# Kernel tuning notes

Measured on AMD Instinct MI355X. Metric: run time of the kernel, lower is better.

Reference implementation:

```python
import jax, jax.numpy as jnp
import numpy as np

B, H, D, E, K = 4096, 1024, 4096, 8, 2


def setup_inputs() -> dict:
    key = jax.random.key(0)
    ks = jax.random.split(key, 7)
    s = 0.02
    return {
        "x": jax.random.normal(ks[0], (B, H), dtype=jnp.float32),
        "gate_w": jax.random.normal(ks[1], (H, E), dtype=jnp.float32) * s,
        "gate_b": jnp.zeros((E,), dtype=jnp.float32),
        "w1": jax.random.normal(ks[2], (E, H, D), dtype=jnp.float32) * s,
        "b1": jnp.zeros((E, D), dtype=jnp.float32),
        "w2": jax.random.normal(ks[3], (E, D, H), dtype=jnp.float32) * s,
        "b2": jnp.zeros((E, H), dtype=jnp.float32),
    }


def reference(x, gate_w, gate_b, w1, b1, w2, b2):
    # Gating: softmax over experts, top-k routing (Switch-style, k=2 here).
    logits = x @ gate_w + gate_b                      # [B, E]
    probs = jax.nn.softmax(logits, axis=-1)           # [B, E]
    topk_vals, topk_idx = jax.lax.top_k(probs, K)     # [B, K]

    # Routing mask: token b routed to expert e iff e in its top-k.
    onehot = jax.nn.one_hot(topk_idx, E, dtype=probs.dtype)  # [B, K, E]
    routed = onehot.max(axis=1)                        # [B, E] in {0,1}

    # Dense per-expert MLPs (grouped GEMM form), then masked scaled combine.
    # h: [E, B, D]; out: [E, B, H]
    h = jax.nn.relu(jnp.einsum('bh,ehd->ebd', x, w1) + b1[:, None, :])
    out = jnp.einsum('ebd,edh->ebh', h, w2) + b2[:, None, :]
    scale = (probs * routed / K).T                     # [E, B]
    y = jnp.einsum('ebh,eb->bh', out, scale)           # [B, H]

    # Switch-style load-balancing aux loss.
    prob_per_expert = probs.mean(axis=0)               # [E]
    tokens_per_expert = routed.mean(axis=0)            # [E]
    aux_loss = (prob_per_expert * tokens_per_expert).sum() * E
    return (y, aux_loss)
```

## Files before the change

### kernel.cpp

```cpp
#include <hip/hip_runtime.h>
#include <stdint.h>
#include <math.h>

typedef unsigned short u16;
typedef __attribute__((ext_vector_type(4))) unsigned short u16x4;
typedef __attribute__((ext_vector_type(8))) short short8;
typedef __attribute__((ext_vector_type(4))) float floatx4;

#define B_TOK 4096
#define H_DIM 1024
#define D_DIM 4096
#define E_NUM 8
#define PAIR_CAP 9216
#define GATE_BLOCKS 256


__device__ __forceinline__ u16 f2bf(float f) {
  union { float f; uint32_t u; } v; v.f = f;
  uint32_t r = (v.u + 0x7fffu + ((v.u >> 16) & 1u)) >> 16;
  return (u16)r;
}

__device__ __forceinline__ void gload_lds16(const u16* g, u16* l) {
  __builtin_amdgcn_global_load_lds((const __attribute__((address_space(1))) void*)g,
                                   (__attribute__((address_space(3))) void*)l, 16, 0, 0);
}


__global__ __launch_bounds__(256) void gate_kernel(
    const float* __restrict__ x, const float* __restrict__ gw, const float* __restrict__ gb,
    int* __restrict__ pcnt, float* __restrict__ psum,
    int* __restrict__ tidx, float* __restrict__ tscale) {
  int wave = threadIdx.x >> 6, lane = threadIdx.x & 63;
  __shared__ int scnt[4][8];
  __shared__ float ssum[4][8];
  int lcnt[8] = {0,0,0,0,0,0,0,0};
  float lsum[8] = {0.f,0.f,0.f,0.f,0.f,0.f,0.f,0.f};

  for (int it = 0; it < 4; it++) {
    int b = blockIdx.x * 16 + it * 4 + wave;
    const float* xr = x + (size_t)b * H_DIM;
    float acc[8] = {0.f,0.f,0.f,0.f,0.f,0.f,0.f,0.f};
    for (int i = 0; i < 16; i++) {
      int h = lane + i * 64;
      float xv = xr[h];
      const float* g = gw + h * 8;
      #pragma unroll
      for (int e = 0; e < 8; e++) acc[e] += xv * g[e];
    }
    #pragma unroll
    for (int e = 0; e < 8; e++) {
      #pragma unroll
      for (int off = 32; off > 0; off >>= 1) acc[e] += __shfl_down(acc[e], off);
    }
    if (lane == 0) {
      float p[8], m = -1e30f, s = 0.f;
      #pragma unroll
      for (int e = 0; e < 8; e++) { p[e] = acc[e] + gb[e]; m = fmaxf(m, p[e]); }
      #pragma unroll
      for (int e = 0; e < 8; e++) { p[e] = expf(p[e] - m); s += p[e]; }
      float inv = 1.f / s;
      #pragma unroll
      for (int e = 0; e < 8; e++) { p[e] *= inv; lsum[e] += p[e]; }
      int i1 = 0;
      #pragma unroll
      for (int e = 1; e < 8; e++) if (p[e] > p[i1]) i1 = e;
      int i2 = (i1 == 0) ? 1 : 0;
      #pragma unroll
      for (int e = 0; e < 8; e++) if (e != i1 && p[e] > p[i2]) i2 = e;
      tidx[2*b]     = i1; tscale[2*b]     = p[i1] * 0.5f;
      tidx[2*b + 1] = i2; tscale[2*b + 1] = p[i2] * 0.5f;
      lcnt[i1]++; lcnt[i2]++;
    }
  }
  if (lane == 0) {
    #pragma unroll
    for (int e = 0; e < 8; e++) { scnt[wave][e] = lcnt[e]; ssum[wave][e] = lsum[e]; }
  }
  __syncthreads();
  if (threadIdx.x < 8) {
    int e = threadIdx.x;
    int c = scnt[0][e] + scnt[1][e] + scnt[2][e] + scnt[3][e];
    float s = ssum[0][e] + ssum[1][e] + ssum[2][e] + ssum[3][e];
    pcnt[blockIdx.x * 8 + e] = c;
    psum[blockIdx.x * 8 + e] = s;
  }
}


__global__ __launch_bounds__(256) void offsets_kernel(
    const int* __restrict__ pcnt, const float* __restrict__ psum,
    int* __restrict__ offs, int* __restrict__ ptok,
    float* __restrict__ pscale, float* __restrict__ aux_out) {
  __shared__ int cnt[8];
  __shared__ float ps[8];
  if (threadIdx.x < 8) {
    int e = threadIdx.x;
    int c = 0; float s = 0.f;
    for (int i = 0; i < GATE_BLOCKS; i++) { c += pcnt[i * 8 + e]; s += psum[i * 8 + e]; }
    cnt[e] = c; ps[e] = s;
  }
  __syncthreads();
  if (threadIdx.x == 0) {
    int o = 0;
    float aux = 0.f;
    for (int e = 0; e < 8; e++) {
      offs[e] = o;
      o += ((cnt[e] + 127) >> 7) << 7;
      aux += (ps[e] * (1.f / 4096.f)) * ((float)cnt[e] * (1.f / 4096.f));
    }
    offs[8] = o;
    aux_out[0] = aux * 8.f;
  }
  for (int i = threadIdx.x; i < PAIR_CAP; i += 256) { ptok[i] = 0; pscale[i] = 0.f; }
}


__global__ __launch_bounds__(256) void scatter_kernel(
    const int* __restrict__ tidx, const float* __restrict__ tscale,
    const int* __restrict__ offs, int* __restrict__ fill,
    int* __restrict__ ptok, float* __restrict__ pscale) {
  __shared__ int lcnt[8];
  __shared__ int lbase[8];
  if (threadIdx.x < 8) lcnt[threadIdx.x] = 0;
  __syncthreads();
  int b = blockIdx.x * 256 + threadIdx.x;
  int e0 = tidx[2*b], e1 = tidx[2*b + 1];
  int p0 = atomicAdd(&lcnt[e0], 1);
  int p1 = atomicAdd(&lcnt[e1], 1);
  __syncthreads();
  if (threadIdx.x < 8) {
    int e = threadIdx.x;
    lbase[e] = offs[e] + atomicAdd(&fill[e], lcnt[e]);
  }
  __syncthreads();
  int pos0 = lbase[e0] + p0;
  int pos1 = lbase[e1] + p1;
  ptok[pos0] = b; pscale[pos0] = tscale[2*b];
  ptok[pos1] = b; pscale[pos1] = tscale[2*b + 1];
}


__global__ __launch_bounds__(256) void convert_x(const float* __restrict__ in, u16* __restrict__ out) {
  int i = blockIdx.x * 256 + threadIdx.x;
  float4 v = ((const float4*)in)[i];
  u16x4 o;
  o[0] = f2bf(v.x); o[1] = f2bf(v.y); o[2] = f2bf(v.z); o[3] = f2bf(v.w);
  ((u16x4*)out)[i] = o;
}


__global__ __launch_bounds__(256) void transpose_convert(
    const float* __restrict__ in, u16* __restrict__ out, int R, int C) {
  __shared__ u16 tile[64 * 65];
  size_t eoff = (size_t)blockIdx.z * R * C;
  const float* inp = in + eoff;
  u16* outp = out + eoff;
  int c0 = blockIdx.x * 64, r0 = blockIdx.y * 64;
  int t = threadIdx.x;
  int rr = t >> 4, cc = t & 15;
  #pragma unroll
  for (int p = 0; p < 4; p++) {
    int r = rr + p * 16;
    float4 v = *(const float4*)(inp + (size_t)(r0 + r) * C + c0 + cc * 4);
    int base = r * 65 + cc * 4;
    tile[base + 0] = f2bf(v.x); tile[base + 1] = f2bf(v.y);
    tile[base + 2] = f2bf(v.z); tile[base + 3] = f2bf(v.w);
  }
  __syncthreads();
  #pragma unroll
  for (int p = 0; p < 4; p++) {
    int c = rr + p * 16;
    u16x4 w;
    w[0] = tile[(cc*4 + 0) * 65 + c];
    w[1] = tile[(cc*4 + 1) * 65 + c];
    w[2] = tile[(cc*4 + 2) * 65 + c];
    w[3] = tile[(cc*4 + 3) * 65 + c];
    *(u16x4*)(outp + (size_t)(c0 + c) * R + r0 + cc * 4) = w;
  }
}


template <bool FIRST>
__global__ __launch_bounds__(256, 2) void moe_gemm(
    const u16* __restrict__ A, const u16* __restrict__ Bw, const float* __restrict__ bias,
    const int* __restrict__ ptok, const float* __restrict__ pscale,
    const int* __restrict__ offs, u16* __restrict__ Hout, float* __restrict__ Y) {
  constexpr int KD = FIRST ? H_DIM : D_DIM;
  constexpr int ND = FIRST ? D_DIM : H_DIM;
  constexpr int AS = FIRST ? H_DIM : D_DIM;

  const int row0 = blockIdx.y * 128;
  const int total = offs[8];
  if (row0 >= total) return;
  int e = 0;
  #pragma unroll
  for (int q = 0; q < 7; q++) if (row0 >= offs[q + 1]) e = q + 1;

  const int n0 = blockIdx.x * 128;
  const int t = threadIdx.x;

  __shared__ __align__(16) u16 lA[128 * 32];
  __shared__ __align__(16) u16 lB[128 * 32];

  const int rA0 = row0 + (t >> 2);
  const int rA1 = rA0 + 64;
  size_t aoff0, aoff1;
  if (FIRST) {
    aoff0 = (size_t)ptok[rA0] * AS;
    aoff1 = (size_t)ptok[rA1] * AS;
  } else {
    aoff0 = (size_t)rA0 * AS;
    aoff1 = (size_t)rA1 * AS;
  }
  const u16* gA0 = A + aoff0 + (t & 3) * 8;
  const u16* gA1 = A + aoff1 + (t & 3) * 8;
  const u16* Be = Bw + (size_t)e * (H_DIM * D_DIM);
  const u16* gB0 = Be + (size_t)(n0 + (t >> 2)) * KD + (t & 3) * 8;
  const u16* gB1 = gB0 + (size_t)64 * KD;
  u16* dA0 = &lA[t * 8];       u16* dA1 = &lA[(t + 256) * 8];
  u16* dB0 = &lB[t * 8];       u16* dB1 = &lB[(t + 256) * 8];

  const int wave = t >> 6, lane = t & 63;
  const int wr = (wave >> 1) * 64, wc = (wave & 1) * 64;
  const int fr = lane & 15, fg = lane >> 4;

  floatx4 acc[4][4];
  #pragma unroll
  for (int i = 0; i < 4; i++)
    #pragma unroll
    for (int j = 0; j < 4; j++) acc[i][j] = (floatx4){0.f, 0.f, 0.f, 0.f};

  for (int k0 = 0; k0 < KD; k0 += 32) {
    gload_lds16(gA0 + k0, dA0);
    gload_lds16(gA1 + k0, dA1);
    gload_lds16(gB0 + k0, dB0);
    gload_lds16(gB1 + k0, dB1);
    __syncthreads();
    short8 af[4], bf[4];
    #pragma unroll
    for (int i = 0; i < 4; i++) af[i] = *(const short8*)&lA[(wr + i * 16 + fr) * 32 + fg * 8];
    #pragma unroll
    for (int j = 0; j < 4; j++) bf[j] = *(const short8*)&lB[(wc + j * 16 + fr) * 32 + fg * 8];
    #pragma unroll
    for (int i = 0; i < 4; i++)
      #pragma unroll
      for (int j = 0; j < 4; j++)
        acc[i][j] = __builtin_amdgcn_mfma_f32_16x16x32_bf16(af[i], bf[j], acc[i][j], 0, 0, 0);
    __syncthreads();
  }

  if (FIRST) {
    const float* be = bias + (size_t)e * ND;
    #pragma unroll
    for (int i = 0; i < 4; i++) {
      #pragma unroll
      for (int r = 0; r < 4; r++) {
        int row = row0 + wr + i * 16 + fg * 4 + r;
        u16* hrow = Hout + (size_t)row * ND;
        #pragma unroll
        for (int j = 0; j < 4; j++) {
          int col = n0 + wc + j * 16 + fr;
          float v = acc[i][j][r] + be[col];
          hrow[col] = f2bf(fmaxf(v, 0.f));
        }
      }
    }
  } else {
    const float* be = bias + (size_t)e * ND;
    #pragma unroll
    for (int i = 0; i < 4; i++) {
      #pragma unroll
      for (int r = 0; r < 4; r++) {
        int row = row0 + wr + i * 16 + fg * 4 + r;
        float sc = pscale[row];
        if (sc != 0.f) {
          int tok = ptok[row];
          float* yrow = Y + (size_t)tok * ND;
          #pragma unroll
          for (int j = 0; j < 4; j++) {
            int col = n0 + wc + j * 16 + fr;
            atomicAdd(&yrow[col], (acc[i][j][r] + be[col]) * sc);
          }
        }
      }
    }
  }
}


extern "C" void kernel_launch(void* const* d_in, const int* in_sizes, int n_in,
                              void* d_out, int out_size, void* d_ws, size_t ws_size,
                              hipStream_t stream) {
  const float* x      = (const float*)d_in[0];
  const float* gate_w = (const float*)d_in[1];
  const float* gate_b = (const float*)d_in[2];
  const float* w1     = (const float*)d_in[3];
  const float* b1     = (const float*)d_in[4];
  const float* w2     = (const float*)d_in[5];
  const float* b2     = (const float*)d_in[6];
  float* out = (float*)d_out;

  char* ws = (char*)d_ws;
  u16*   x_bf   = (u16*)  (ws);
  u16*   w1t    = (u16*)  (ws + 8388608);
  u16*   w2t    = (u16*)  (ws + 75497472);
  u16*   h_bf   = (u16*)  (ws + 142606336);
  int*   ptok   = (int*)  (ws + 218103808);
  float* pscale = (float*)(ws + 218140672);
  int*   tidx   = (int*)  (ws + 218177536);
  float* tscale = (float*)(ws + 218210304);
  int*   ctr    = (int*)  (ws + 218243072);
  int*   fill     = ctr;
  int*   offs     = ctr + 8;
  int*   pcnt     = ctr + 32;
  float* psum     = (float*)(ctr + 32 + GATE_BLOCKS * 8);

  hipMemsetAsync(d_out, 0, (size_t)out_size * sizeof(float), stream);
  hipMemsetAsync(fill, 0, 8 * sizeof(int), stream);

  convert_x<<<(B_TOK * H_DIM) / 4 / 256, 256, 0, stream>>>(x, x_bf);
  transpose_convert<<<dim3(D_DIM / 64, H_DIM / 64, E_NUM), 256, 0, stream>>>(w1, w1t, H_DIM, D_DIM);
  transpose_convert<<<dim3(H_DIM / 64, D_DIM / 64, E_NUM), 256, 0, stream>>>(w2, w2t, D_DIM, H_DIM);
  gate_kernel<<<GATE_BLOCKS, 256, 0, stream>>>(x, gate_w, gate_b, pcnt, psum, tidx, tscale);
  offsets_kernel<<<1, 256, 0, stream>>>(pcnt, psum, offs, ptok, pscale, out + (size_t)B_TOK * H_DIM);
  scatter_kernel<<<B_TOK / 256, 256, 0, stream>>>(tidx, tscale, offs, fill, ptok, pscale);
  moe_gemm<true><<<dim3(D_DIM / 128, PAIR_CAP / 128), 256, 0, stream>>>(
      x_bf, w1t, b1, ptok, pscale, offs, h_bf, nullptr);
  moe_gemm<false><<<dim3(H_DIM / 128, PAIR_CAP / 128), 256, 0, stream>>>(
      h_bf, w2t, b2, ptok, pscale, offs, nullptr, out);
}
```

Baseline: 617.7 us.

## Split-K second GEMM into per-pair partials, add swizzled LDS, deterministic combine

The second expert GEMM now splits K into two halves across blockIdx.z and writes plain fp32 partial results per routed pair into a workspace buffer, rather than doing scaled atomicAdds into the output. A new combine kernel gathers each token's two pairs and both K-halves, adds the bias and applies the routing scales. This doubles the grid for the small-N second GEMM and removes the atomics and the output memset. An XOR swizzle on the LDS tile column is also added to cut bank conflicts in both GEMMs. The cost is extra partial-buffer traffic, about 75MB written and read back, which reuses the x_bf/w1t region of the workspace.

```diff
diff --git a/kernel.cpp b/kernel.cpp
--- a/kernel.cpp
+++ b/kernel.cpp
@@ -90,8 +90,7 @@
 
 __global__ __launch_bounds__(256) void offsets_kernel(
     const int* __restrict__ pcnt, const float* __restrict__ psum,
-    int* __restrict__ offs, int* __restrict__ ptok,
-    float* __restrict__ pscale, float* __restrict__ aux_out) {
+    int* __restrict__ offs, int* __restrict__ ptok, float* __restrict__ aux_out) {
   __shared__ int cnt[8];
   __shared__ float ps[8];
   if (threadIdx.x < 8) {
@@ -112,14 +111,15 @@
     offs[8] = o;
     aux_out[0] = aux * 8.f;
   }
-  for (int i = threadIdx.x; i < PAIR_CAP; i += 256) { ptok[i] = 0; pscale[i] = 0.f; }
+  for (int i = threadIdx.x; i < PAIR_CAP; i += 256) ptok[i] = 0;
 }
 
 
 __global__ __launch_bounds__(256) void scatter_kernel(
     const int* __restrict__ tidx, const float* __restrict__ tscale,
     const int* __restrict__ offs, int* __restrict__ fill,
-    int* __restrict__ ptok, float* __restrict__ pscale) {
+    int* __restrict__ ptok, float* __restrict__ pscale,
+    int* __restrict__ pexp, int* __restrict__ pairpos) {
   __shared__ int lcnt[8];
   __shared__ int lbase[8];
   if (threadIdx.x < 8) lcnt[threadIdx.x] = 0;
@@ -136,8 +136,8 @@
   __syncthreads();
   int pos0 = lbase[e0] + p0;
   int pos1 = lbase[e1] + p1;
-  ptok[pos0] = b; pscale[pos0] = tscale[2*b];
-  ptok[pos1] = b; pscale[pos1] = tscale[2*b + 1];
+  ptok[pos0] = b; pscale[pos0] = tscale[2*b];     pexp[pos0] = e0; pairpos[2*b]     = pos0;
+  ptok[pos1] = b; pscale[pos1] = tscale[2*b + 1]; pexp[pos1] = e1; pairpos[2*b + 1] = pos1;
 }
 
 
@@ -184,9 +184,10 @@
 template <bool FIRST>
 __global__ __launch_bounds__(256, 2) void moe_gemm(
     const u16* __restrict__ A, const u16* __restrict__ Bw, const float* __restrict__ bias,
-    const int* __restrict__ ptok, const float* __restrict__ pscale,
-    const int* __restrict__ offs, u16* __restrict__ Hout, float* __restrict__ Y) {
+    const int* __restrict__ ptok, const int* __restrict__ offs,
+    u16* __restrict__ Hout, float* __restrict__ Y) {
   constexpr int KD = FIRST ? H_DIM : D_DIM;
+  constexpr int KSPAN = FIRST ? KD : KD / 2;
   constexpr int ND = FIRST ? D_DIM : H_DIM;
   constexpr int AS = FIRST ? H_DIM : D_DIM;
 
@@ -199,6 +200,7 @@
 
   const int n0 = blockIdx.x * 128;
   const int t = threadIdx.x;
+  const int kbase = FIRST ? 0 : (int)blockIdx.z * KSPAN;
 
   __shared__ __align__(16) u16 lA[128 * 32];
   __shared__ __align__(16) u16 lB[128 * 32];
@@ -213,10 +215,11 @@
     aoff0 = (size_t)rA0 * AS;
     aoff1 = (size_t)rA1 * AS;
   }
-  const u16* gA0 = A + aoff0 + (t & 3) * 8;
-  const u16* gA1 = A + aoff1 + (t & 3) * 8;
+  const int kc = (((t & 3) ^ ((t >> 3) & 3))) * 8;
+  const u16* gA0 = A + aoff0 + kbase + kc;
+  const u16* gA1 = A + aoff1 + kbase + kc;
   const u16* Be = Bw + (size_t)e * (H_DIM * D_DIM);
-  const u16* gB0 = Be + (size_t)(n0 + (t >> 2)) * KD + (t & 3) * 8;
+  const u16* gB0 = Be + (size_t)(n0 + (t >> 2)) * KD + kbase + kc;
   const u16* gB1 = gB0 + (size_t)64 * KD;
   u16* dA0 = &lA[t * 8];       u16* dA1 = &lA[(t + 256) * 8];
   u16* dB0 = &lB[t * 8];       u16* dB1 = &lB[(t + 256) * 8];
@@ -224,6 +227,7 @@
   const int wave = t >> 6, lane = t & 63;
   const int wr = (wave >> 1) * 64, wc = (wave & 1) * 64;
   const int fr = lane & 15, fg = lane >> 4;
+  const int sw = (fg ^ ((fr >> 1) & 3)) * 8;
 
   floatx4 acc[4][4];
   #pragma unroll
@@ -231,7 +235,7 @@
     #pragma unroll
     for (int j = 0; j < 4; j++) acc[i][j] = (floatx4){0.f, 0.f, 0.f, 0.f};
 
-  for (int k0 = 0; k0 < KD; k0 += 32) {
+  for (int k0 = 0; k0 < KSPAN; k0 += 32) {
     gload_lds16(gA0 + k0, dA0);
     gload_lds16(gA1 + k0, dA1);
     gload_lds16(gB0 + k0, dB0);
@@ -239,9 +243,9 @@
     __syncthreads();
     short8 af[4], bf[4];
     #pragma unroll
-    for (int i = 0; i < 4; i++) af[i] = *(const short8*)&lA[(wr + i * 16 + fr) * 32 + fg * 8];
-    #pragma unroll
-    for (int j = 0; j < 4; j++) bf[j] = *(const short8*)&lB[(wc + j * 16 + fr) * 32 + fg * 8];
+    for (int i = 0; i < 4; i++) af[i] = *(const short8*)&lA[(wr + i * 16 + fr) * 32 + sw];
+    #pragma unroll
+    for (int j = 0; j < 4; j++) bf[j] = *(const short8*)&lB[(wc + j * 16 + fr) * 32 + sw];
     #pragma unroll
     for (int i = 0; i < 4; i++)
       #pragma unroll
@@ -267,25 +271,45 @@
       }
     }
   } else {
-    const float* be = bias + (size_t)e * ND;
+    float* yp = Y + (size_t)blockIdx.z * ((size_t)PAIR_CAP * H_DIM);
     #pragma unroll
     for (int i = 0; i < 4; i++) {
       #pragma unroll
       for (int r = 0; r < 4; r++) {
         int row = row0 + wr + i * 16 + fg * 4 + r;
-        float sc = pscale[row];
-        if (sc != 0.f) {
-          int tok = ptok[row];
-          float* yrow = Y + (size_t)tok * ND;
-          #pragma unroll
-          for (int j = 0; j < 4; j++) {
-            int col = n0 + wc + j * 16 + fr;
-            atomicAdd(&yrow[col], (acc[i][j][r] + be[col]) * sc);
-          }
+        float* yrow = yp + (size_t)row * ND;
+        #pragma unroll
+        for (int j = 0; j < 4; j++) {
+          int col = n0 + wc + j * 16 + fr;
+          yrow[col] = acc[i][j][r];
         }
       }
     }
   }
+}
+
+
+__global__ __launch_bounds__(256) void combine_kernel(
+    const float* __restrict__ yp, const int* __restrict__ pairpos,
+    const float* __restrict__ pscale, const int* __restrict__ pexp,
+    const float* __restrict__ b2, float* __restrict__ y) {
+  const size_t SS = (size_t)PAIR_CAP * H_DIM;
+  int tok = blockIdx.x;
+  int c = threadIdx.x * 4;
+  int p0 = pairpos[2 * tok], p1 = pairpos[2 * tok + 1];
+  float s0 = pscale[p0], s1 = pscale[p1];
+  float4 a0 = *(const float4*)(yp + (size_t)p0 * H_DIM + c);
+  float4 a1 = *(const float4*)(yp + SS + (size_t)p0 * H_DIM + c);
+  float4 a2 = *(const float4*)(yp + (size_t)p1 * H_DIM + c);
+  float4 a3 = *(const float4*)(yp + SS + (size_t)p1 * H_DIM + c);
+  float4 q0 = *(const float4*)(b2 + (size_t)pexp[p0] * H_DIM + c);
+  float4 q1 = *(const float4*)(b2 + (size_t)pexp[p1] * H_DIM + c);
+  float4 r;
+  r.x = s0 * (a0.x + a1.x + q0.x) + s1 * (a2.x + a3.x + q1.x);
+  r.y = s0 * (a0.y + a1.y + q0.y) + s1 * (a2.y + a3.y + q1.y);
+  r.z = s0 * (a0.z + a1.z + q0.z) + s1 * (a2.z + a3.z + q1.z);
+  r.w = s0 * (a0.w + a1.w + q0.w) + s1 * (a2.w + a3.w + q1.w);
+  *(float4*)(y + (size_t)tok * H_DIM + c) = r;
 }
 
 
@@ -304,6 +328,7 @@
   char* ws = (char*)d_ws;
   u16*   x_bf   = (u16*)  (ws);
   u16*   w1t    = (u16*)  (ws + 8388608);
+  float* ypair  = (float*)(ws);
   u16*   w2t    = (u16*)  (ws + 75497472);
   u16*   h_bf   = (u16*)  (ws + 142606336);
   int*   ptok   = (int*)  (ws + 218103808);
@@ -315,18 +340,20 @@
   int*   offs     = ctr + 8;
   int*   pcnt     = ctr + 32;
   float* psum     = (float*)(ctr + 32 + GATE_BLOCKS * 8);
-
-  hipMemsetAsync(d_out, 0, (size_t)out_size * sizeof(float), stream);
+  int*   pairpos  = (int*)  (ws + 218300416);
+  int*   pexp     = (int*)  (ws + 218333184);
+
   hipMemsetAsync(fill, 0, 8 * sizeof(int), stream);
 
   convert_x<<<(B_TOK * H_DIM) / 4 / 256, 256, 0, stream>>>(x, x_bf);
   transpose_convert<<<dim3(D_DIM / 64, H_DIM / 64, E_NUM), 256, 0, stream>>>(w1, w1t, H_DIM, D_DIM);
   transpose_convert<<<dim3(H_DIM / 64, D_DIM / 64, E_NUM), 256, 0, stream>>>(w2, w2t, D_DIM, H_DIM);
   gate_kernel<<<GATE_BLOCKS, 256, 0, stream>>>(x, gate_w, gate_b, pcnt, psum, tidx, tscale);
-  offsets_kernel<<<1, 256, 0, stream>>>(pcnt, psum, offs, ptok, pscale, out + (size_t)B_TOK * H_DIM);
-  scatter_kernel<<<B_TOK / 256, 256, 0, stream>>>(tidx, tscale, offs, fill, ptok, pscale);
-  moe_gemm<true><<<dim3(D_DIM / 128, PAIR_CAP / 128), 256, 0, stream>>>(
-      x_bf, w1t, b1, ptok, pscale, offs, h_bf, nullptr);
-  moe_gemm<false><<<dim3(H_DIM / 128, PAIR_CAP / 128), 256, 0, stream>>>(
-      h_bf, w2t, b2, ptok, pscale, offs, nullptr, out);
-}
+  offsets_kernel<<<1, 256, 0, stream>>>(pcnt, psum, offs, ptok, out + (size_t)B_TOK * H_DIM);
+  scatter_kernel<<<B_TOK / 256, 256, 0, stream>>>(tidx, tscale, offs, fill, ptok, pscale, pexp, pairpos);
+  moe_gemm<true><<<dim3(D_DIM / 128, PAIR_CAP / 128, 1), 256, 0, stream>>>(
+      x_bf, w1t, b1, ptok, offs, h_bf, nullptr);
+  moe_gemm<false><<<dim3(H_DIM / 128, PAIR_CAP / 128, 2), 256, 0, stream>>>(
+      h_bf, w2t, nullptr, ptok, offs, nullptr, ypair);
+  combine_kernel<<<B_TOK, 256, 0, stream>>>(ypair, pairpos, pscale, pexp, b2, out);
+}
```

New measurement: 610.3 us. About the same (-1.2%).
